# Optimization experiments

Measured on AMD Instinct MI355X. Metric: run time of the kernel, lower is better.

Reference implementation:

```python
import jax, jax.numpy as jnp
import numpy as np

N = 20000      # atoms
E = 320000     # pairs (avg degree 16)
F = 64         # per-atom features
NRBF = 32      # radial basis functions
RC = 1.0       # maximum_interaction_radius


def _decompose(t):
    # X = I + A + S (irreducible decomposition of 3x3 tensors)
    diag_mean = jnp.diagonal(t, axis1=-2, axis2=-1).mean(-1)
    I = diag_mean[..., None, None] * jnp.eye(3, dtype=t.dtype)
    A = 0.5 * (t - jnp.swapaxes(t, -1, -2))
    S = 0.5 * (t + jnp.swapaxes(t, -1, -2)) - I
    return I, A, S


def _tnorm(t):
    # Frobenius norm^2 over the trailing 3x3 -> [N, F]
    return (t ** 2).sum((-2, -1))


def _lin_t(t, W):
    # channel-mixing linear on the feature axis of [N, F, 3, 3]
    return jnp.einsum('nfij,gf->ngij', t, W)


def setup_inputs():
    key = jax.random.key(0)
    ks = jax.random.split(key, 14)
    inp = {
        'X': jax.random.normal(ks[0], (N, F, 3, 3), jnp.float32) * 0.1,
        'pair_indices': jax.random.randint(ks[1], (2, E), 0, N, jnp.int32),
        'd_ij': jax.random.uniform(ks[2], (E, 1), jnp.float32),
        'radial_feature_vector': jax.random.normal(ks[3], (E, NRBF), jnp.float32),
        'atomic_charges': jax.random.normal(ks[4], (N,), jnp.float32) * 0.1,
        # mlp_scalar: NRBF -> F -> 2F -> 3F (Dense = Linear + activation)
        'W0': jax.random.normal(ks[5], (F, NRBF), jnp.float32) / np.sqrt(NRBF),
        'b0': jnp.zeros((F,), jnp.float32),
        'W1': jax.random.normal(ks[6], (2 * F, F), jnp.float32) / np.sqrt(F),
        'b1': jnp.zeros((2 * F,), jnp.float32),
        'W2': jax.random.normal(ks[7], (3 * F, 2 * F), jnp.float32) / np.sqrt(2 * F),
        'b2': jnp.zeros((3 * F,), jnp.float32),
        # 6 bias-free FxF tensor linears
        'Wt': jax.random.normal(ks[8], (6, F, F), jnp.float32) / np.sqrt(F),
    }
    return inp


def reference(X, pair_indices, d_ij, radial_feature_vector, atomic_charges,
              W0, b0, W1, b1, W2, b2, Wt):
    silu = jax.nn.silu
    n_atoms = X.shape[0]
    src = pair_indices[1]  # gathered
    dst = pair_indices[0]  # scattered (index_add_)

    # cosine cutoff, [E, 1]
    C = (0.5 * (jnp.cos(jnp.pi * d_ij / RC) + 1.0)
         * (d_ij < RC).astype(X.dtype)).reshape(-1, 1)

    h = silu(radial_feature_vector @ W0.T + b0)
    h = silu(h @ W1.T + b1)
    h = silu(h @ W2.T + b2)                 # [E, 3F]
    rfv = (h * C).reshape(-1, F, 3)          # [E, F, 3]

    X = X / (_tnorm(X) + 1.0)[..., None, None]
    I, A, S = _decompose(X)
    I = _lin_t(I, Wt[0])
    A = _lin_t(A, Wt[1])
    S = _lin_t(S, Wt[2])
    Y = I + A + S

    def mp(r, T):
        # gather-mul-scatter: [E,F,3,3] messages reduced to [N,F,3,3]
        msg = r[:, :, None, None] * T[src]
        return jax.ops.segment_sum(msg, dst, num_segments=n_atoms)

    msg = mp(rfv[..., 0], I) + mp(rfv[..., 1], A) + mp(rfv[..., 2], S)

    # O(3) group
    q = (1.0 + 0.1 * atomic_charges)[:, None, None, None]
    I, A, S = _decompose(q * (jnp.matmul(msg, Y) + jnp.matmul(Y, msg)))

    normp1 = (_tnorm(I + A + S) + 1.0)[..., None, None]
    I, A, S = I / normp1, A / normp1, S / normp1
    I = _lin_t(I, Wt[3])
    A = _lin_t(A, Wt[4])
    S = _lin_t(S, Wt[5])
    dX = I + A + S

    X = X + dX + q * jnp.matmul(dX, dX)
    return X
```

## Files before the change

kernel.cpp:

```cpp
#include <hip/hip_runtime.h>
#include <hip/hip_bf16.h>
#include <cmath>

#define N_ATOMS 20000
#define NE      320000
#define FDIM    64
#define NRBF    32
#define PI_F    3.14159265358979323846f

typedef __attribute__((ext_vector_type(8))) short bf16x8;
typedef __attribute__((ext_vector_type(4))) float f32x4;

#define MFMA16(a, b, c) __builtin_amdgcn_mfma_f32_16x16x32_bf16(a, b, c, 0, 0, 0)

__device__ __forceinline__ float silu(float x) {
    return x / (1.0f + __expf(-x));
}

__device__ __forceinline__ unsigned short f2bf_rne(float x) {
    unsigned u = __float_as_uint(x);
    u += 0x7fffu + ((u >> 16) & 1u);
    return (unsigned short)(u >> 16);
}

__device__ __forceinline__ void split8(const float* v, bf16x8& hi, bf16x8& lo) {
#pragma unroll
    for (int j = 0; j < 8; j++) {
        unsigned u = __float_as_uint(v[j]);
        float hf = __uint_as_float(u & 0xffff0000u);
        hi[j] = (short)(u >> 16);
        lo[j] = (short)f2bf_rne(v[j] - hf);
    }
}

__global__ void transpose_kernel(const float* __restrict__ Wt, float* __restrict__ wtT) {
    int idx = blockIdx.x * 256 + threadIdx.x;
    if (idx >= 24576) return;
    int k = idx >> 12;
    int r = idx & 4095;
    int g = r >> 6;
    int f = r & 63;
    wtT[k * 4096 + f * 64 + g] = Wt[idx];
}

__global__ void wfrag_kernel(const float* __restrict__ W0, const float* __restrict__ W1,
                             const float* __restrict__ W2,
                             unsigned short* __restrict__ f0h, unsigned short* __restrict__ f0l,
                             unsigned short* __restrict__ f1h, unsigned short* __restrict__ f1l,
                             unsigned short* __restrict__ f2h, unsigned short* __restrict__ f2l) {
    int idx = blockIdx.x * 256 + threadIdx.x;
    const float* W;
    unsigned short *fh, *fl;
    int t, K, NT;
    if (idx < 2048)       { W = W0; fh = f0h; fl = f0l; t = idx;         K = 32;  NT = 4; }
    else if (idx < 10240) { W = W1; fh = f1h; fl = f1l; t = idx - 2048;  K = 64;  NT = 8; }
    else if (idx < 34816) { W = W2; fh = f2h; fl = f2l; t = idx - 10240; K = 128; NT = 12; }
    else return;
    int j = t & 7;
    int lane = (t >> 3) & 63;
    int rest = t >> 9;
    int nt = rest % NT;
    int ks = rest / NT;
    int k = ks * 32 + ((lane >> 4) & 3) * 8 + j;
    int n = nt * 16 + (lane & 15);
    float w = W[n * K + k];
    unsigned u = __float_as_uint(w);
    float hf = __uint_as_float(u & 0xffff0000u);
    fh[t] = (unsigned short)(u >> 16);
    fl[t] = f2bf_rne(w - hf);
}

__global__ void hist_kernel(const int* __restrict__ dst, int* __restrict__ deg) {
    int e = blockIdx.x * 256 + threadIdx.x;
    if (e >= NE) return;
    atomicAdd(&deg[dst[e]], 1);
}

__global__ void scan_kernel(const int* __restrict__ deg, int* __restrict__ off) {
    __shared__ int part[1024];
    int t = threadIdx.x;
    const int CH = (N_ATOMS + 1023) / 1024;
    int base = t * CH;
    int s = 0;
    for (int i = 0; i < CH; i++) {
        int idx = base + i;
        if (idx < N_ATOMS) s += deg[idx];
    }
    part[t] = s;
    __syncthreads();
    for (int ofs = 1; ofs < 1024; ofs <<= 1) {
        int v = (t >= ofs) ? part[t - ofs] : 0;
        __syncthreads();
        part[t] += v;
        __syncthreads();
    }
    int run = (t == 0) ? 0 : part[t - 1];
    for (int i = 0; i < CH; i++) {
        int idx = base + i;
        if (idx < N_ATOMS) {
            off[idx] = run;
            run += deg[idx];
        }
    }
    if (t == 1023) off[N_ATOMS] = run;
}

__global__ void fill_kernel(const int* __restrict__ dst, const int* __restrict__ srcArr,
                            const int* __restrict__ off, int* __restrict__ cursor,
                            int2* __restrict__ esbkt) {
    int e = blockIdx.x * 256 + threadIdx.x;
    if (e >= NE) return;
    int d = dst[e];
    int pos = atomicAdd(&cursor[d], 1);
    esbkt[off[d] + pos] = make_int2(e, srcArr[e]);
}

#define H1S 68
#define H2S 132
__global__ __launch_bounds__(128) void mlp_mfma_kernel(
    const float* __restrict__ rfv, const float* __restrict__ dij,
    const float* __restrict__ b0, const float* __restrict__ b1, const float* __restrict__ b2,
    const unsigned short* __restrict__ f0h, const unsigned short* __restrict__ f0l,
    const unsigned short* __restrict__ f1h, const unsigned short* __restrict__ f1l,
    const unsigned short* __restrict__ f2h, const unsigned short* __restrict__ f2l,
    __hip_bfloat16* __restrict__ r) {
    __shared__ float h1s[2][32][H1S];
    __shared__ float h2s[2][32][H2S];
    const int w = threadIdx.x >> 6;
    const int lane = threadIdx.x & 63;
    const int q = lane >> 4;
    const int c = lane & 15;
    const int e0 = (blockIdx.x * 2 + w) * 32;
    float (*h1)[H1S] = h1s[w];
    float (*h2)[H2S] = h2s[w];

    {
        bf16x8 ah[2], al[2];
#pragma unroll
        for (int mt = 0; mt < 2; mt++) {
            float v[8];
            const float* p = rfv + (size_t)(e0 + mt * 16 + c) * 32 + q * 8;
            *(float4*)(v)     = *(const float4*)(p);
            *(float4*)(v + 4) = *(const float4*)(p + 4);
            split8(v, ah[mt], al[mt]);
        }
#pragma unroll
        for (int nt = 0; nt < 4; nt++) {
            float bias = b0[nt * 16 + c];
            f32x4 acc[2];
            acc[0] = {bias, bias, bias, bias};
            acc[1] = acc[0];
            bf16x8 bh = *(const bf16x8*)(f0h + (size_t)(nt * 64 + lane) * 8);
            bf16x8 bl = *(const bf16x8*)(f0l + (size_t)(nt * 64 + lane) * 8);
#pragma unroll
            for (int mt = 0; mt < 2; mt++) {
                acc[mt] = MFMA16(al[mt], bh, acc[mt]);
                acc[mt] = MFMA16(ah[mt], bl, acc[mt]);
                acc[mt] = MFMA16(ah[mt], bh, acc[mt]);
            }
#pragma unroll
            for (int mt = 0; mt < 2; mt++)
#pragma unroll
                for (int reg = 0; reg < 4; reg++)
                    h1[mt * 16 + q * 4 + reg][nt * 16 + c] = silu(acc[mt][reg]);
        }
    }

    {
        bf16x8 ah[2][2], al[2][2];
#pragma unroll
        for (int mt = 0; mt < 2; mt++)
#pragma unroll
            for (int ks = 0; ks < 2; ks++) {
                float v[8];
                const float* p = &h1[mt * 16 + c][ks * 32 + q * 8];
                *(float4*)(v)     = *(const float4*)(p);
                *(float4*)(v + 4) = *(const float4*)(p + 4);
                split8(v, ah[mt][ks], al[mt][ks]);
            }
#pragma unroll
        for (int nt = 0; nt < 8; nt++) {
            float bias = b1[nt * 16 + c];
            f32x4 acc[2];
            acc[0] = {bias, bias, bias, bias};
            acc[1] = acc[0];
#pragma unroll
            for (int ks = 0; ks < 2; ks++) {
                bf16x8 bh = *(const bf16x8*)(f1h + (size_t)((ks * 8 + nt) * 64 + lane) * 8);
                bf16x8 bl = *(const bf16x8*)(f1l + (size_t)((ks * 8 + nt) * 64 + lane) * 8);
#pragma unroll
                for (int mt = 0; mt < 2; mt++) {
                    acc[mt] = MFMA16(al[mt][ks], bh, acc[mt]);
                    acc[mt] = MFMA16(ah[mt][ks], bl, acc[mt]);
                    acc[mt] = MFMA16(ah[mt][ks], bh, acc[mt]);
                }
            }
#pragma unroll
            for (int mt = 0; mt < 2; mt++)
#pragma unroll
                for (int reg = 0; reg < 4; reg++)
                    h2[mt * 16 + q * 4 + reg][nt * 16 + c] = silu(acc[mt][reg]);
        }
    }

    {
        bf16x8 ah[2][4], al[2][4];
#pragma unroll
        for (int mt = 0; mt < 2; mt++)
#pragma unroll
            for (int ks = 0; ks < 4; ks++) {
                float v[8];
                const float* p = &h2[mt * 16 + c][ks * 32 + q * 8];
                *(float4*)(v)     = *(const float4*)(p);
                *(float4*)(v + 4) = *(const float4*)(p + 4);
                split8(v, ah[mt][ks], al[mt][ks]);
            }
        float cut[2][4];
#pragma unroll
        for (int mt = 0; mt < 2; mt++)
#pragma unroll
            for (int reg = 0; reg < 4; reg++) {
                float d = dij[e0 + mt * 16 + q * 4 + reg];
                cut[mt][reg] = (d < 1.0f) ? 0.5f * (__cosf(PI_F * d) + 1.0f) : 0.0f;
            }
#pragma unroll
        for (int nt = 0; nt < 12; nt++) {
            float bias = b2[nt * 16 + c];
            f32x4 acc[2];
            acc[0] = {bias, bias, bias, bias};
            acc[1] = acc[0];
#pragma unroll
            for (int ks = 0; ks < 4; ks++) {
                bf16x8 bh = *(const bf16x8*)(f2h + (size_t)((ks * 12 + nt) * 64 + lane) * 8);
                bf16x8 bl = *(const bf16x8*)(f2l + (size_t)((ks * 12 + nt) * 64 + lane) * 8);
#pragma unroll
                for (int mt = 0; mt < 2; mt++) {
                    acc[mt] = MFMA16(al[mt][ks], bh, acc[mt]);
                    acc[mt] = MFMA16(ah[mt][ks], bl, acc[mt]);
                    acc[mt] = MFMA16(ah[mt][ks], bh, acc[mt]);
                }
            }
#pragma unroll
            for (int mt = 0; mt < 2; mt++)
#pragma unroll
                for (int reg = 0; reg < 4; reg++)
                    r[(size_t)(e0 + mt * 16 + q * 4 + reg) * 192 + nt * 16 + c] =
                        __float2bfloat16(silu(acc[mt][reg]) * cut[mt][reg]);
        }
    }
}

__global__ __launch_bounds__(256) void lin1_kernel(
    const float* __restrict__ X, const float* __restrict__ wtT,
    float* __restrict__ comp, float* __restrict__ Yb) {
    __shared__ float lds[4][64 * 11];
    int w = threadIdx.x >> 6;
    int l = threadIdx.x & 63;
    int a = blockIdx.x * 4 + w;

    {
        const float* x = X + ((size_t)a * 64 + l) * 9;
        float v[9];
#pragma unroll
        for (int i = 0; i < 9; i++) v[i] = x[i];
        float t2 = 0.f;
#pragma unroll
        for (int i = 0; i < 9; i++) t2 += v[i] * v[i];
        float inv = 1.0f / (t2 + 1.0f);
#pragma unroll
        for (int i = 0; i < 9; i++) v[i] *= inv;
        float iso = (v[0] + v[4] + v[8]) * (1.0f / 3.0f);
        float* o = &lds[w][l * 11];
        o[0] = iso;
        o[1] = 0.5f * (v[1] - v[3]);
        o[2] = 0.5f * (v[2] - v[6]);
        o[3] = 0.5f * (v[5] - v[7]);
        o[4] = v[0] - iso;
        o[5] = 0.5f * (v[1] + v[3]);
        o[6] = 0.5f * (v[2] + v[6]);
        o[7] = v[4] - iso;
        o[8] = 0.5f * (v[5] + v[7]);
        o[9] = v[8] - iso;
    }
    __syncthreads();
    {
        int g = l;
        const float* w0 = wtT;
        const float* w1 = wtT + 4096;
        const float* w2 = wtT + 8192;
        float acc[10];
#pragma unroll
        for (int c = 0; c < 10; c++) acc[c] = 0.f;
        for (int f = 0; f < 64; f++) {
            float wI = w0[f * 64 + g];
            float wA = w1[f * 64 + g];
            float wS = w2[f * 64 + g];
            const float* rf = &lds[w][f * 11];
            acc[0] += wI * rf[0];
            acc[1] += wA * rf[1];
            acc[2] += wA * rf[2];
            acc[3] += wA * rf[3];
#pragma unroll
            for (int c = 4; c < 10; c++) acc[c] += wS * rf[c];
        }
        float* co = comp + ((size_t)a * 64 + g) * 12;
        float4 c0 = {acc[0], acc[1], acc[2], acc[3]};
        float4 c1 = {acc[4], acc[5], acc[6], acc[7]};
        float4 c2 = {acc[8], acc[9], 0.f, 0.f};
        *(float4*)(co)     = c0;
        *(float4*)(co + 4) = c1;
        *(float4*)(co + 8) = c2;
        float* y = Yb + ((size_t)a * 64 + g) * 9;
        y[0] = acc[0] + acc[4];
        y[1] = acc[5] + acc[1];
        y[2] = acc[6] + acc[2];
        y[3] = acc[5] - acc[1];
        y[4] = acc[0] + acc[7];
        y[5] = acc[8] + acc[3];
        y[6] = acc[6] - acc[2];
        y[7] = acc[8] - acc[3];
        y[8] = acc[0] + acc[9];
    }
}

__global__ __launch_bounds__(256) void msg_lin2_kernel(
    const int* __restrict__ off, const int2* __restrict__ esbkt,
    const __hip_bfloat16* __restrict__ r,
    const float* __restrict__ comp, const float* __restrict__ Yb,
    const float* __restrict__ X, const float* __restrict__ charges,
    const float* __restrict__ wtT, float* __restrict__ out) {
    __shared__ float lds[4][64 * 11];
    int w = threadIdx.x >> 6;
    int l = threadIdx.x & 63;
    int a = blockIdx.x * 4 + w;
    float q = 1.0f + 0.1f * charges[a];

    float m[10];
#pragma unroll
    for (int c = 0; c < 10; c++) m[c] = 0.f;
    {
        int beg = off[a], end = off[a + 1];
        for (int i = beg; i < end; i++) {
            int2 es = esbkt[i];
            const __hip_bfloat16* rp = r + (size_t)es.x * 192 + l * 3;
            float r0 = __bfloat162float(rp[0]);
            float r1 = __bfloat162float(rp[1]);
            float r2 = __bfloat162float(rp[2]);
            const float* cp = comp + ((size_t)es.y * 64 + l) * 12;
            float4 c0 = *(const float4*)(cp);
            float4 c1 = *(const float4*)(cp + 4);
            float4 c2 = *(const float4*)(cp + 8);
            m[0] += r0 * c0.x;
            m[1] += r1 * c0.y;
            m[2] += r1 * c0.z;
            m[3] += r1 * c0.w;
            m[4] += r2 * c1.x;
            m[5] += r2 * c1.y;
            m[6] += r2 * c1.z;
            m[7] += r2 * c1.w;
            m[8] += r2 * c2.x;
            m[9] += r2 * c2.y;
        }
    }

    {
        float M[9];
        M[0] = m[0] + m[4]; M[1] = m[5] + m[1]; M[2] = m[6] + m[2];
        M[3] = m[5] - m[1]; M[4] = m[0] + m[7]; M[5] = m[8] + m[3];
        M[6] = m[6] - m[2]; M[7] = m[8] - m[3]; M[8] = m[0] + m[9];
        const float* yp = Yb + ((size_t)a * 64 + l) * 9;
        float Y[9];
#pragma unroll
        for (int i = 0; i < 9; i++) Y[i] = yp[i];
        float P[9];
#pragma unroll
        for (int i = 0; i < 3; i++) {
#pragma unroll
            for (int j = 0; j < 3; j++) {
                float s = 0.f;
#pragma unroll
                for (int k = 0; k < 3; k++)
                    s += M[i * 3 + k] * Y[k * 3 + j] + Y[i * 3 + k] * M[k * 3 + j];
                P[i * 3 + j] = q * s;
            }
        }
        float t2 = 0.f;
#pragma unroll
        for (int i = 0; i < 9; i++) t2 += P[i] * P[i];
        float inv = 1.0f / (t2 + 1.0f);
        float iso = (P[0] + P[4] + P[8]) * (1.0f / 3.0f);
        float* o = &lds[w][l * 11];
        o[0] = iso * inv;
        o[1] = 0.5f * (P[1] - P[3]) * inv;
        o[2] = 0.5f * (P[2] - P[6]) * inv;
        o[3] = 0.5f * (P[5] - P[7]) * inv;
        o[4] = (P[0] - iso) * inv;
        o[5] = 0.5f * (P[1] + P[3]) * inv;
        o[6] = 0.5f * (P[2] + P[6]) * inv;
        o[7] = (P[4] - iso) * inv;
        o[8] = 0.5f * (P[5] + P[7]) * inv;
        o[9] = (P[8] - iso) * inv;
    }
    __syncthreads();
    {
        int g = l;
        const float* w3 = wtT + 3 * 4096;
        const float* w4 = wtT + 4 * 4096;
        const float* w5 = wtT + 5 * 4096;
        float acc[10];
#pragma unroll
        for (int c = 0; c < 10; c++) acc[c] = 0.f;
        for (int f = 0; f < 64; f++) {
            float wI = w3[f * 64 + g];
            float wA = w4[f * 64 + g];
            float wS = w5[f * 64 + g];
            const float* rf = &lds[w][f * 11];
            acc[0] += wI * rf[0];
            acc[1] += wA * rf[1];
            acc[2] += wA * rf[2];
            acc[3] += wA * rf[3];
#pragma unroll
            for (int c = 4; c < 10; c++) acc[c] += wS * rf[c];
        }
        float D[9];
        D[0] = acc[0] + acc[4]; D[1] = acc[5] + acc[1]; D[2] = acc[6] + acc[2];
        D[3] = acc[5] - acc[1]; D[4] = acc[0] + acc[7]; D[5] = acc[8] + acc[3];
        D[6] = acc[6] - acc[2]; D[7] = acc[8] - acc[3]; D[8] = acc[0] + acc[9];

        const float* x = X + ((size_t)a * 64 + g) * 9;
        float xv[9];
#pragma unroll
        for (int i = 0; i < 9; i++) xv[i] = x[i];
        float t2 = 0.f;
#pragma unroll
        for (int i = 0; i < 9; i++) t2 += xv[i] * xv[i];
        float invn = 1.0f / (t2 + 1.0f);
#pragma unroll
        for (int i = 0; i < 9; i++) xv[i] *= invn;

        float DD[9];
#pragma unroll
        for (int i = 0; i < 3; i++) {
#pragma unroll
            for (int j = 0; j < 3; j++) {
                float s = 0.f;
#pragma unroll
                for (int k = 0; k < 3; k++) s += D[i * 3 + k] * D[k * 3 + j];
                DD[i * 3 + j] = s;
            }
        }
        float* op = out + ((size_t)a * 64 + g) * 9;
#pragma unroll
        for (int i = 0; i < 9; i++) op[i] = xv[i] + D[i] + q * DD[i];
    }
}

extern "C" void kernel_launch(void* const* d_in, const int* in_sizes, int n_in,
                              void* d_out, int out_size, void* d_ws, size_t ws_size,
                              hipStream_t stream) {
    const float* X       = (const float*)d_in[0];
    const int*   pair    = (const int*)d_in[1];
    const float* dij     = (const float*)d_in[2];
    const float* rfv     = (const float*)d_in[3];
    const float* charges = (const float*)d_in[4];
    const float* W0      = (const float*)d_in[5];
    const float* b0      = (const float*)d_in[6];
    const float* W1      = (const float*)d_in[7];
    const float* b1      = (const float*)d_in[8];
    const float* W2      = (const float*)d_in[9];
    const float* b2      = (const float*)d_in[10];
    const float* Wt      = (const float*)d_in[11];
    float* out = (float*)d_out;

    const int* dst = pair;
    const int* src = pair + NE;

    char* ws = (char*)d_ws;
    size_t ofs = 0;
    auto alloc = [&](size_t bytes) {
        void* p = ws + ofs;
        ofs += (bytes + 255) & ~(size_t)255;
        return p;
    };
    float* wtT  = (float*)alloc((size_t)6 * 4096 * 4);
    unsigned short* f0h = (unsigned short*)alloc(2048 * 2);
    unsigned short* f0l = (unsigned short*)alloc(2048 * 2);
    unsigned short* f1h = (unsigned short*)alloc(8192 * 2);
    unsigned short* f1l = (unsigned short*)alloc(8192 * 2);
    unsigned short* f2h = (unsigned short*)alloc(24576 * 2);
    unsigned short* f2l = (unsigned short*)alloc(24576 * 2);
    float* comp = (float*)alloc((size_t)N_ATOMS * FDIM * 12 * 4);
    __hip_bfloat16* rbuf = (__hip_bfloat16*)alloc((size_t)NE * 192 * 2);
    int* deg    = (int*)alloc((size_t)N_ATOMS * 4);
    int* offarr = (int*)alloc((size_t)(N_ATOMS + 1) * 4);
    int* cursor = (int*)alloc((size_t)N_ATOMS * 4);
    int2* esbkt = (int2*)alloc((size_t)NE * 8);
    float* Yb   = out;

    hipMemsetAsync(deg, 0, (size_t)N_ATOMS * 4, stream);
    hipMemsetAsync(cursor, 0, (size_t)N_ATOMS * 4, stream);

    transpose_kernel<<<(24576 + 255) / 256, 256, 0, stream>>>(Wt, wtT);
    wfrag_kernel<<<(34816 + 255) / 256, 256, 0, stream>>>(
        W0, W1, W2, f0h, f0l, f1h, f1l, f2h, f2l);
    hist_kernel<<<NE / 256, 256, 0, stream>>>(dst, deg);
    scan_kernel<<<1, 1024, 0, stream>>>(deg, offarr);
    fill_kernel<<<NE / 256, 256, 0, stream>>>(dst, src, offarr, cursor, esbkt);

    mlp_mfma_kernel<<<NE / 64, 128, 0, stream>>>(
        rfv, dij, b0, b1, b2, f0h, f0l, f1h, f1l, f2h, f2l, rbuf);

    lin1_kernel<<<N_ATOMS / 4, 256, 0, stream>>>(X, wtT, comp, Yb);

    msg_lin2_kernel<<<N_ATOMS / 4, 256, 0, stream>>>(
        offarr, esbkt, rbuf, comp, Yb, X, charges, wtT, out);
}
```

Before: 561.7 us.

## Write edge MLP output in dst-sorted order and prefetch gathers in message loop

The MLP kernel now scatters each edge's radial-weight row to its CSR slot, so the message kernel reads r contiguously by slot instead of gathering by edge id. The bucket array shrinks to source indices only. The message loop is software-pipelined so the next edge's loads are issued before the current accumulation. In exchange, the MLP's stores become scattered rows, and the extra registers for prefetched values may lower occupancy.

```diff
diff --git a/kernel.cpp b/kernel.cpp
--- a/kernel.cpp
+++ b/kernel.cpp
@@ -107,12 +107,14 @@
 
 __global__ void fill_kernel(const int* __restrict__ dst, const int* __restrict__ srcArr,
                             const int* __restrict__ off, int* __restrict__ cursor,
-                            int2* __restrict__ esbkt) {
+                            int* __restrict__ sbkt, int* __restrict__ slotOf) {
     int e = blockIdx.x * 256 + threadIdx.x;
     if (e >= NE) return;
     int d = dst[e];
     int pos = atomicAdd(&cursor[d], 1);
-    esbkt[off[d] + pos] = make_int2(e, srcArr[e]);
+    int slot = off[d] + pos;
+    sbkt[slot] = srcArr[e];
+    slotOf[e] = slot;
 }
 
 #define H1S 68
@@ -123,6 +125,7 @@
     const unsigned short* __restrict__ f0h, const unsigned short* __restrict__ f0l,
     const unsigned short* __restrict__ f1h, const unsigned short* __restrict__ f1l,
     const unsigned short* __restrict__ f2h, const unsigned short* __restrict__ f2l,
+    const int* __restrict__ slotOf,
     __hip_bfloat16* __restrict__ r) {
     __shared__ float h1s[2][32][H1S];
     __shared__ float h2s[2][32][H2S];
@@ -216,12 +219,15 @@
                 split8(v, ah[mt][ks], al[mt][ks]);
             }
         float cut[2][4];
+        int srow[2][4];
 #pragma unroll
         for (int mt = 0; mt < 2; mt++)
 #pragma unroll
             for (int reg = 0; reg < 4; reg++) {
-                float d = dij[e0 + mt * 16 + q * 4 + reg];
+                int e = e0 + mt * 16 + q * 4 + reg;
+                float d = dij[e];
                 cut[mt][reg] = (d < 1.0f) ? 0.5f * (__cosf(PI_F * d) + 1.0f) : 0.0f;
+                srow[mt][reg] = slotOf[e];
             }
 #pragma unroll
         for (int nt = 0; nt < 12; nt++) {
@@ -244,7 +250,7 @@
             for (int mt = 0; mt < 2; mt++)
 #pragma unroll
                 for (int reg = 0; reg < 4; reg++)
-                    r[(size_t)(e0 + mt * 16 + q * 4 + reg) * 192 + nt * 16 + c] =
+                    r[(size_t)srow[mt][reg] * 192 + nt * 16 + c] =
                         __float2bfloat16(silu(acc[mt][reg]) * cut[mt][reg]);
         }
     }
@@ -324,7 +330,7 @@
 }
 
 __global__ __launch_bounds__(256) void msg_lin2_kernel(
-    const int* __restrict__ off, const int2* __restrict__ esbkt,
+    const int* __restrict__ off, const int* __restrict__ sbkt,
     const __hip_bfloat16* __restrict__ r,
     const float* __restrict__ comp, const float* __restrict__ Yb,
     const float* __restrict__ X, const float* __restrict__ charges,
@@ -340,16 +346,43 @@
     for (int c = 0; c < 10; c++) m[c] = 0.f;
     {
         int beg = off[a], end = off[a + 1];
-        for (int i = beg; i < end; i++) {
-            int2 es = esbkt[i];
-            const __hip_bfloat16* rp = r + (size_t)es.x * 192 + l * 3;
-            float r0 = __bfloat162float(rp[0]);
-            float r1 = __bfloat162float(rp[1]);
-            float r2 = __bfloat162float(rp[2]);
-            const float* cp = comp + ((size_t)es.y * 64 + l) * 12;
-            float4 c0 = *(const float4*)(cp);
-            float4 c1 = *(const float4*)(cp + 4);
-            float4 c2 = *(const float4*)(cp + 8);
+        if (beg < end) {
+            __hip_bfloat16 ra, rb, rc;
+            float4 c0, c1, c2;
+            {
+                const __hip_bfloat16* rp = r + (size_t)beg * 192 + l * 3;
+                ra = rp[0]; rb = rp[1]; rc = rp[2];
+                const float* cp = comp + ((size_t)sbkt[beg] * 64 + l) * 12;
+                c0 = *(const float4*)(cp);
+                c1 = *(const float4*)(cp + 4);
+                c2 = *(const float4*)(cp + 8);
+            }
+            for (int i = beg + 1; i < end; i++) {
+                const __hip_bfloat16* rp = r + (size_t)i * 192 + l * 3;
+                __hip_bfloat16 na = rp[0], nb = rp[1], nc = rp[2];
+                const float* cp = comp + ((size_t)sbkt[i] * 64 + l) * 12;
+                float4 n0 = *(const float4*)(cp);
+                float4 n1 = *(const float4*)(cp + 4);
+                float4 n2 = *(const float4*)(cp + 8);
+                float r0 = __bfloat162float(ra);
+                float r1 = __bfloat162float(rb);
+                float r2 = __bfloat162float(rc);
+                m[0] += r0 * c0.x;
+                m[1] += r1 * c0.y;
+                m[2] += r1 * c0.z;
+                m[3] += r1 * c0.w;
+                m[4] += r2 * c1.x;
+                m[5] += r2 * c1.y;
+                m[6] += r2 * c1.z;
+                m[7] += r2 * c1.w;
+                m[8] += r2 * c2.x;
+                m[9] += r2 * c2.y;
+                ra = na; rb = nb; rc = nc;
+                c0 = n0; c1 = n1; c2 = n2;
+            }
+            float r0 = __bfloat162float(ra);
+            float r1 = __bfloat162float(rb);
+            float r2 = __bfloat162float(rc);
             m[0] += r0 * c0.x;
             m[1] += r1 * c0.y;
             m[2] += r1 * c0.z;
@@ -494,7 +527,8 @@
     int* deg    = (int*)alloc((size_t)N_ATOMS * 4);
     int* offarr = (int*)alloc((size_t)(N_ATOMS + 1) * 4);
     int* cursor = (int*)alloc((size_t)N_ATOMS * 4);
-    int2* esbkt = (int2*)alloc((size_t)NE * 8);
+    int* sbkt   = (int*)alloc((size_t)NE * 4);
+    int* slotOf = (int*)alloc((size_t)NE * 4);
     float* Yb   = out;
 
     hipMemsetAsync(deg, 0, (size_t)N_ATOMS * 4, stream);
@@ -505,13 +539,13 @@
         W0, W1, W2, f0h, f0l, f1h, f1l, f2h, f2l);
     hist_kernel<<<NE / 256, 256, 0, stream>>>(dst, deg);
     scan_kernel<<<1, 1024, 0, stream>>>(deg, offarr);
-    fill_kernel<<<NE / 256, 256, 0, stream>>>(dst, src, offarr, cursor, esbkt);
+    fill_kernel<<<NE / 256, 256, 0, stream>>>(dst, src, offarr, cursor, sbkt, slotOf);
 
     mlp_mfma_kernel<<<NE / 64, 128, 0, stream>>>(
-        rfv, dij, b0, b1, b2, f0h, f0l, f1h, f1l, f2h, f2l, rbuf);
+        rfv, dij, b0, b1, b2, f0h, f0l, f1h, f1l, f2h, f2l, slotOf, rbuf);
 
     lin1_kernel<<<N_ATOMS / 4, 256, 0, stream>>>(X, wtT, comp, Yb);
 
     msg_lin2_kernel<<<N_ATOMS / 4, 256, 0, stream>>>(
-        offarr, esbkt, rbuf, comp, Yb, X, charges, wtT, out);
-}
+        offarr, sbkt, rbuf, comp, Yb, X, charges, wtT, out);
+}
```

Result: no change. 553.8 us (-1.4%).
